# Performance work log

Measured on AMD Instinct MI355X. Metric: run time of the kernel, lower is better.

Reference implementation:

```python
import jax, jax.numpy as jnp
import numpy as np

NB_LAYERS, KSIZE = 4, 5
DILATIONS = [1, 2, 4, 8]
NEG_SLOPE = 0.1
BN_EPS = 1e-5


def _cont_conv(times, feats, mask, dilation, p):
    """One ContConv1d layer: causal gather of time-diffs -> kernel MLP -> weighted aggregate + skip + BN."""
    k1W, k1b, k2W, k2b, k3W, k3b, skipW, skipb, gamma, beta = p
    bs, L, Cin = feats.shape
    Cout = skipW.shape[1]
    lags = jnp.arange(KSIZE) * dilation                    # (K,) include_zero_lag=True -> lag 0 included
    idx = jnp.arange(L)[None, :] - lags[:, None]           # (K, L) causal neighbor indices
    valid = idx >= 0
    idx_c = jnp.clip(idx, 0, L - 1)
    g_times = times[:, idx_c]                              # (bs, K, L)
    g_feats = feats[:, idx_c, :]                           # (bs, K, L, Cin)
    g_mask = (mask[:, idx_c] & valid[None] & mask[:, None, :]).astype(feats.dtype)
    dt = (times[:, None, :] - g_times) * g_mask            # (bs, K, L) zeroed where invalid
    # kernel MLP: scalar time-diff -> (Cin, Cout) mixing matrix
    h = jax.nn.leaky_relu(dt[..., None] @ k1W + k1b, NEG_SLOPE)
    h = jax.nn.leaky_relu(h @ k2W + k2b, NEG_SLOPE)
    kv = (h @ k3W + k3b).reshape(bs, KSIZE, L, Cin, Cout) * g_mask[..., None, None]
    out = jnp.einsum('bklc,bklcd->bld', g_feats, kv)       # aggregate over taps and input channels
    out = out + feats @ skipW + skipb                      # 1x1-conv skip connection
    mu = out.mean((0, 1))                                  # BatchNorm1d (training-mode batch stats)
    var = out.var((0, 1))
    return (out - mu) * jax.lax.rsqrt(var + BN_EPS) * gamma + beta


def _ccnn_forward(event_times, event_types, emb, k1W, k1b, k2W, k2b, k3W, k3b, skipW, skipb, gamma, beta):
    bs = event_times.shape[0]
    emb = emb.at[0].set(0.0)                               # padding_idx = 0
    times = jnp.concatenate([jnp.zeros((bs, 1), event_times.dtype), event_times], axis=1)
    bos = jnp.full((bs, 1), jnp.max(event_types) + 1, dtype=event_types.dtype)
    types = jnp.concatenate([bos, event_types], axis=1)
    mask = times != 0                                      # BOS (t=0) masked, as in the original
    enc = emb[types]                                       # (bs, L+1, C)
    for i in range(NB_LAYERS):
        p = (k1W[i], k1b[i], k2W[i], k2b[i], k3W[i], k3b[i], skipW[i], skipb[i], gamma[i], beta[i])
        enc = jax.nn.leaky_relu(_cont_conv(times, enc, mask, DILATIONS[i], p), NEG_SLOPE)
    return enc


def setup_inputs() -> dict:
    key = jax.random.key(0)
    ks = jax.random.split(key, 12)
    bs, L, C, H, num_types = 8, 2048, 32, 16, 100
    s = 0.05
    gaps = jax.random.uniform(ks[0], (bs, L)) * 0.1 + 0.01
    times = jnp.cumsum(gaps, axis=1)                       # strictly increasing positive event times
    types = jax.random.randint(ks[1], (bs, L), 0, num_types) + 1   # 1..num_types
    pad = jnp.arange(L) >= int(0.9 * L)
    times = jnp.where(pad[None, :], 0.0, times).astype(jnp.float32)
    types = jnp.where(pad[None, :], 0, types).astype(jnp.int32)
    return {
        'event_times': times,
        'event_types': types,
        'emb': jax.random.normal(ks[2], (num_types + 2, C)) * s,
        'k1W': jax.random.normal(ks[3], (NB_LAYERS, 1, H)) * s,
        'k1b': jnp.zeros((NB_LAYERS, H)),
        'k2W': jax.random.normal(ks[4], (NB_LAYERS, H, H)) * s,
        'k2b': jnp.zeros((NB_LAYERS, H)),
        'k3W': jax.random.normal(ks[5], (NB_LAYERS, H, C * C)) * s,
        'k3b': jnp.zeros((NB_LAYERS, C * C)),
        'skipW': jax.random.normal(ks[6], (NB_LAYERS, C, C)) * s,
        'skipb': jnp.zeros((NB_LAYERS, C)),
        'gamma': jnp.ones((NB_LAYERS, C)),
        'beta': jnp.zeros((NB_LAYERS, C)),
    }


def reference(event_times, event_types, emb, k1W, k1b, k2W, k2b, k3W, k3b, skipW, skipb, gamma, beta):
    return _ccnn_forward(event_times, event_types, emb, k1W, k1b, k2W, k2b, k3W, k3b, skipW, skipb, gamma, beta)
```

## Files before the change

### kernel.cpp

```cpp
#include <hip/hip_runtime.h>
#include <stdint.h>

#define NB_LAYERS 4
#define KSIZE 5
#define BSZ 8
#define LIN 2048
#define LSEQ 2049
#define CCH 32
#define HCH 16
#define MROWS (BSZ*LSEQ)
#define NTILES ((MROWS+15)/16)
#define NEG 0.1f
#define BNEPS 1e-5f
#define CONVGRID 205
#define CONVBLK 320
#define NFRAG 36
#define WT_HALVES (NFRAG*64*8)

typedef _Float16 h2v __attribute__((ext_vector_type(2)));
typedef _Float16 h8v __attribute__((ext_vector_type(8)));
typedef float    f4v __attribute__((ext_vector_type(4)));

union H8 { h8v v; h2v h[4]; };

static __device__ __forceinline__ h2v mkh2(float a, float b) {
  h2v r; r[0] = (_Float16)a; r[1] = (_Float16)b; return r;
}

static __device__ __forceinline__ void wt_decode(
    int g, const float* __restrict__ k3Wl, const float* __restrict__ k3bl,
    const float* __restrict__ skipWl, int& halfidx, float& val) {
  int n, k;
  if (g < 16384)      { n = g & 31; int c = (g >> 5) & 31; int h = g >> 10; k = h * 32 + c; val = k3Wl[g]; }
  else if (g < 17408) { int g2 = g - 16384; n = g2 & 31; int c = g2 >> 5; k = 512 + c; val = k3bl[g2]; }
  else                { int g2 = g - 17408; n = g2 & 31; int c = g2 >> 5; k = 544 + c; val = skipWl[g2]; }
  int m = n & 15, a = n >> 4, qq = (k >> 3) & 3, hh = k & 7;
  int f = (k < 512) ? ((k >> 5) * 2 + a) : ((k < 544) ? (32 + a) : (34 + a));
  halfidx = f * 512 + ((qq << 4) | m) * 8 + hh;
}

template<int MODE>
__global__ __launch_bounds__(CONVBLK) void conv_kernel(
    const float* __restrict__ enc_in,
    const int*   __restrict__ types,
    const float* __restrict__ emb,
    float* __restrict__ enc_out,
    const float* __restrict__ etimes,
    const float* __restrict__ k1Wp, const float* __restrict__ k1bp,
    const float* __restrict__ k2Wp, const float* __restrict__ k2bp,
    const float* __restrict__ k3W, const float* __restrict__ k3b,
    const float* __restrict__ skipW,
    _Float16* __restrict__ WtG,
    const float* __restrict__ stats_prev,
    const float* __restrict__ partials_prev,
    float* __restrict__ stats_out,
    float* __restrict__ partials_out,
    float* __restrict__ stats_zero,
    const float* __restrict__ gamma_prev, const float* __restrict__ beta_prev,
    int dil)
{
  __shared__ h8v Wl[NFRAG * 64];
  __shared__ h8v swh[(CONVBLK/64) * KSIZE * 16 * 2];
  __shared__ alignas(16) float sW[304];
  __shared__ float sst[64];
  __shared__ float sbn[64];

  const int tid  = threadIdx.x;
  const int lane = tid & 63;
  const int wv   = tid >> 6;
  const int m    = lane & 15;
  const int q    = lane >> 4;

  if (tid < 64) sst[tid] = 0.f;
  if (tid < 16) { sW[tid] = k1Wp[tid]; sW[16 + tid] = k1bp[tid]; sW[32 + tid] = k2bp[tid]; }
  if (tid >= 64) sW[48 + tid - 64] = k2Wp[tid - 64];

  if (MODE == 0) {
    if (blockIdx.x == 0 && tid < 192) stats_zero[tid] = 0.f;
    for (int g = tid; g < WT_HALVES; g += CONVBLK) {
      int hi; float val;
      wt_decode(g, k3W, k3b, skipW, hi, val);
      ((_Float16*)Wl)[hi] = (_Float16)val;
    }
    int id2 = blockIdx.x * CONVBLK + tid;
    if (id2 < 3 * WT_HALVES) {
      int layer = 1 + id2 / WT_HALVES;
      int g = id2 - (layer - 1) * WT_HALVES;
      int hi; float val;
      wt_decode(g, k3W + layer * 16384, k3b + layer * 1024, skipW + layer * 1024, hi, val);
      WtG[(layer - 1) * WT_HALVES + hi] = (_Float16)val;
    }
  } else {
    const float4* src = (const float4*)WtG;
    float4* dst = (float4*)Wl;
    for (int i = tid; i < WT_HALVES / 8; i += CONVBLK) dst[i] = src[i];
    if (partials_prev && tid < 64) sbn[tid] = 0.f;
  }
  __syncthreads();

  if (MODE == 1 && partials_prev) {
    float v = 0.f;
    for (int i = tid; i < CONVGRID * 64; i += CONVBLK) v += partials_prev[i];
    atomicAdd(&sbn[tid & 63], v);
    __syncthreads();
  }

  float sc8[8], ob8[8];
  if (MODE == 1) {
    const float inv = 1.f / (float)MROWS;
#pragma unroll
    for (int j = 0; j < 8; j++) {
      int c = q * 8 + j;
      float s1 = partials_prev ? sbn[c]      : stats_prev[c];
      float s2 = partials_prev ? sbn[32 + c] : stats_prev[32 + c];
      float mu = s1 * inv;
      float var = s2 * inv - mu * mu;
      float sc = gamma_prev[c] * rsqrtf(var + BNEPS);
      sc8[j] = sc; ob8[j] = beta_prev[c] - mu * sc;
    }
  }

  const int tile = blockIdx.x * (CONVBLK / 64) + wv;
  int row = tile * 16 + m;
  bool rvalid = row < MROWS;
  int rowc = min(row, MROWS - 1);
  int b = rowc / LSEQ, pos = rowc % LSEQ;
  float t_l = (pos == 0) ? 0.f : etimes[b * LIN + pos - 1];
  bool mask_l = rvalid && (t_l != 0.f);

  int bosv = 0;
  if (MODE == 0) {
    if (__ballot(pos == 0)) {
      int mx = 0;
#pragma unroll 8
      for (int i = lane; i < BSZ * LIN; i += 64) mx = max(mx, types[i]);
#pragma unroll
      for (int off = 32; off; off >>= 1) mx = max(mx, __shfl_xor(mx, off, 64));
      bosv = mx + 1;
    }
  }

  int jcs[KSIZE]; float tjv[KSIZE];
#pragma unroll
  for (int tap = 0; tap < KSIZE; tap++) {
    int j = pos - tap * dil;
    int jc = max(j, 0); jcs[tap] = jc;
    tjv[tap] = (jc == 0) ? 0.f : etimes[b * LIN + jc - 1];
  }
  float4 fa[KSIZE], fbv[KSIZE];
  int tts[KSIZE];
  if (MODE == 0) {
#pragma unroll
    for (int tap = 0; tap < KSIZE; tap++) {
      int jc = jcs[tap];
      tts[tap] = (jc > 0) ? types[b * LIN + jc - 1] : ((tap == 0) ? bosv : 0);
    }
#pragma unroll
    for (int tap = 0; tap < KSIZE; tap++) {
      const float* ep = emb + tts[tap] * CCH + q * 8;
      fa[tap] = *(const float4*)ep; fbv[tap] = *(const float4*)(ep + 4);
    }
  } else {
#pragma unroll
    for (int tap = 0; tap < KSIZE; tap++) {
      const float* fp = enc_in + (b * LSEQ + jcs[tap]) * CCH + q * 8;
      fa[tap] = *(const float4*)fp; fbv[tap] = *(const float4*)(fp + 4);
    }
  }

  h2v fh[KSIZE][4];
  h2v fself[4];
  float Fb[8];
#pragma unroll
  for (int jj = 0; jj < 8; jj++) Fb[jj] = 0.f;

#pragma unroll
  for (int tap = 0; tap < KSIZE; tap++) {
    bool gm = mask_l && (pos - tap * dil >= 0) && (tjv[tap] != 0.f);
    float fv[8] = {fa[tap].x, fa[tap].y, fa[tap].z, fa[tap].w,
                   fbv[tap].x, fbv[tap].y, fbv[tap].z, fbv[tap].w};
    if (MODE == 0) {
      float zf = (tts[tap] != 0) ? 1.f : 0.f;
#pragma unroll
      for (int jj = 0; jj < 8; jj++) fv[jj] *= zf;
    } else {
#pragma unroll
      for (int jj = 0; jj < 8; jj++) {
        float x = fmaf(fv[jj], sc8[jj], ob8[jj]);
        fv[jj] = fmaxf(x, NEG * x);
      }
    }
    if (tap == 0) {
      float rv = rvalid ? 1.f : 0.f;
#pragma unroll
      for (int p2 = 0; p2 < 4; p2++) fself[p2] = mkh2(fv[2*p2] * rv, fv[2*p2+1] * rv);
    }
    float g = gm ? 1.f : 0.f;
#pragma unroll
    for (int jj = 0; jj < 8; jj++) Fb[jj] += g * fv[jj];
#pragma unroll
    for (int p2 = 0; p2 < 4; p2++) fh[tap][p2] = mkh2(fv[2*p2], fv[2*p2+1]);
  }

#pragma unroll
  for (int rep = 0; rep < 2; rep++) {
    const int jt = rep ? (KSIZE - 1) : (lane >> 4);
    const bool act = rep ? (lane < 16) : true;
    int j2 = pos - jt * dil;
    int jc2 = max(j2, 0);
    float tj2 = (jc2 == 0) ? 0.f : etimes[b * LIN + jc2 - 1];
    bool g2 = act && mask_l && (j2 >= 0) && (tj2 != 0.f);
    float dt = g2 ? (t_l - tj2) : 0.f;

    H8 w0, w1;
    if (__ballot(g2)) {
      const f4v* k1wv = (const f4v*)&sW[0];
      const f4v* k1bv = (const f4v*)&sW[16];
      const f4v* k2bv = (const f4v*)&sW[32];
      float h1[HCH], h2[HCH];
#pragma unroll
      for (int h4 = 0; h4 < 4; h4++) {
        f4v cw = k1wv[h4], cb = k1bv[h4], c2 = k2bv[h4];
#pragma unroll
        for (int r = 0; r < 4; r++) {
          float x = fmaf(dt, cw[r], cb[r]);
          h1[h4*4+r] = fmaxf(x, NEG * x);
          h2[h4*4+r] = c2[r];
        }
      }
#pragma unroll
      for (int hp = 0; hp < HCH; hp++) {
        float hv = h1[hp];
        const f4v* kk = (const f4v*)&sW[48 + hp * 16];
#pragma unroll
        for (int h4 = 0; h4 < 4; h4++) {
          f4v c = kk[h4];
#pragma unroll
          for (int r = 0; r < 4; r++) h2[h4*4+r] = fmaf(hv, c[r], h2[h4*4+r]);
        }
      }
      float g = g2 ? 1.f : 0.f;
#pragma unroll
      for (int p2 = 0; p2 < 4; p2++) {
        float a0 = h2[2*p2];     a0 = fmaxf(a0, NEG * a0) * g;
        float a1 = h2[2*p2+1];   a1 = fmaxf(a1, NEG * a1) * g;
        w0.h[p2] = mkh2(a0, a1);
        float b0 = h2[8+2*p2];   b0 = fmaxf(b0, NEG * b0) * g;
        float b1 = h2[8+2*p2+1]; b1 = fmaxf(b1, NEG * b1) * g;
        w1.h[p2] = mkh2(b0, b1);
      }
    } else {
#pragma unroll
      for (int p2 = 0; p2 < 4; p2++) { w0.h[p2] = mkh2(0.f, 0.f); w1.h[p2] = mkh2(0.f, 0.f); }
    }
    if (act) {
      int base = ((wv * KSIZE + jt) * 16 + m) * 2;
      swh[base] = w0.v; swh[base + 1] = w1.v;
    }
  }
  __syncthreads();

  h2v wh[KSIZE][8];
#pragma unroll
  for (int tap = 0; tap < KSIZE; tap++) {
    int base = ((wv * KSIZE + tap) * 16 + m) * 2;
    H8 a0, a1; a0.v = swh[base]; a1.v = swh[base + 1];
#pragma unroll
    for (int p2 = 0; p2 < 4; p2++) { wh[tap][p2] = a0.h[p2]; wh[tap][4+p2] = a1.h[p2]; }
  }

  f4v aP = {0,0,0,0}, aQ = {0,0,0,0}, bP = {0,0,0,0}, bQ = {0,0,0,0};

#pragma unroll
  for (int ks = 0; ks < 16; ks++) {
    H8 bf0, bf1, af;
    bf0.v = Wl[(2*ks + 0) * 64 + lane];
    bf1.v = Wl[(2*ks + 1) * 64 + lane];
    h2v u0 = mkh2(0.f,0.f), u1 = mkh2(0.f,0.f), u2 = mkh2(0.f,0.f), u3 = mkh2(0.f,0.f);
#pragma unroll
    for (int tap = 0; tap < KSIZE; tap++) {
      _Float16 w = wh[tap][ks >> 1][ks & 1];
      h2v wd; wd[0] = w; wd[1] = w;
      u0 += wd * fh[tap][0];
      u1 += wd * fh[tap][1];
      u2 += wd * fh[tap][2];
      u3 += wd * fh[tap][3];
    }
    af.h[0] = u0; af.h[1] = u1; af.h[2] = u2; af.h[3] = u3;
    if (ks & 1) {
      aQ = __builtin_amdgcn_mfma_f32_16x16x32_f16(af.v, bf0.v, aQ, 0, 0, 0);
      bQ = __builtin_amdgcn_mfma_f32_16x16x32_f16(af.v, bf1.v, bQ, 0, 0, 0);
    } else {
      aP = __builtin_amdgcn_mfma_f32_16x16x32_f16(af.v, bf0.v, aP, 0, 0, 0);
      bP = __builtin_amdgcn_mfma_f32_16x16x32_f16(af.v, bf1.v, bP, 0, 0, 0);
    }
  }
  {
    H8 bf0, bf1, af;
    bf0.v = Wl[32 * 64 + lane];
    bf1.v = Wl[33 * 64 + lane];
#pragma unroll
    for (int p2 = 0; p2 < 4; p2++) af.h[p2] = mkh2(Fb[2*p2], Fb[2*p2+1]);
    aP = __builtin_amdgcn_mfma_f32_16x16x32_f16(af.v, bf0.v, aP, 0, 0, 0);
    bP = __builtin_amdgcn_mfma_f32_16x16x32_f16(af.v, bf1.v, bP, 0, 0, 0);
  }
  {
    H8 bf0, bf1, af;
    bf0.v = Wl[34 * 64 + lane];
    bf1.v = Wl[35 * 64 + lane];
    af.h[0] = fself[0]; af.h[1] = fself[1]; af.h[2] = fself[2]; af.h[3] = fself[3];
    aQ = __builtin_amdgcn_mfma_f32_16x16x32_f16(af.v, bf0.v, aQ, 0, 0, 0);
    bQ = __builtin_amdgcn_mfma_f32_16x16x32_f16(af.v, bf1.v, bQ, 0, 0, 0);
  }
  f4v acc0 = aP + aQ;
  f4v acc1 = bP + bQ;

  float s0 = 0.f, s1 = 0.f, s2 = 0.f, s3 = 0.f;
#pragma unroll
  for (int r = 0; r < 4; r++) {
    float v0 = acc0[r], v1 = acc1[r];
    s0 += v0; s1 += v0 * v0; s2 += v1; s3 += v1 * v1;
    int rd = tile * 16 + q * 4 + r;
    if (rd < MROWS) {
      enc_out[rd * CCH + m] = v0;
      enc_out[rd * CCH + 16 + m] = v1;
    }
  }
  s0 += __shfl_xor(s0, 16, 64); s0 += __shfl_xor(s0, 32, 64);
  s1 += __shfl_xor(s1, 16, 64); s1 += __shfl_xor(s1, 32, 64);
  s2 += __shfl_xor(s2, 16, 64); s2 += __shfl_xor(s2, 32, 64);
  s3 += __shfl_xor(s3, 16, 64); s3 += __shfl_xor(s3, 32, 64);
  if (q == 0) {
    atomicAdd(&sst[m], s0);
    atomicAdd(&sst[32 + m], s1);
    atomicAdd(&sst[16 + m], s2);
    atomicAdd(&sst[48 + m], s3);
  }
  __syncthreads();
  if (tid < 64) {
    if (MODE == 0) partials_out[blockIdx.x * 64 + tid] = sst[tid];
    else           atomicAdd(&stats_out[tid], sst[tid]);
  }
}

__global__ __launch_bounds__(256) void bn_kernel(
    const float* __restrict__ x, float* __restrict__ out,
    const float* __restrict__ stats,
    const float* __restrict__ gamma, const float* __restrict__ beta) {
  int id = blockIdx.x * blockDim.x + threadIdx.x;
  int c = id & 31;
  const float inv = 1.f / (float)MROWS;
  float mu = stats[c] * inv;
  float var = stats[32 + c] * inv - mu * mu;
  float sc = gamma[c] * rsqrtf(var + BNEPS);
  float v = fmaf(x[id], sc, beta[c] - mu * sc);
  out[id] = fmaxf(v, NEG * v);
}

extern "C" void kernel_launch(void* const* d_in, const int* in_sizes, int n_in,
                              void* d_out, int out_size, void* d_ws, size_t ws_size,
                              hipStream_t stream) {
  (void)in_sizes; (void)n_in; (void)out_size; (void)ws_size;
  const float* event_times = (const float*)d_in[0];
  const int*   event_types = (const int*)d_in[1];
  const float* emb   = (const float*)d_in[2];
  const float* k1W   = (const float*)d_in[3];
  const float* k1b   = (const float*)d_in[4];
  const float* k2W   = (const float*)d_in[5];
  const float* k2b   = (const float*)d_in[6];
  const float* k3W   = (const float*)d_in[7];
  const float* k3b   = (const float*)d_in[8];
  const float* skipW = (const float*)d_in[9];
  const float* gamma = (const float*)d_in[11];
  const float* beta  = (const float*)d_in[12];

  float* enc_a = (float*)d_ws;
  float* enc_b = enc_a + (size_t)MROWS * CCH;
  float* stats = enc_b + (size_t)MROWS * CCH;
  float* partials0 = stats + NB_LAYERS * 64;
  _Float16* WtG = (_Float16*)(((uintptr_t)(partials0 + CONVGRID * 64) + 255) & ~(uintptr_t)255);

  conv_kernel<0><<<CONVGRID, CONVBLK, 0, stream>>>(
      nullptr, event_types, emb, enc_b, event_times,
      k1W, k1b, k2W, k2b, k3W, k3b, skipW, WtG,
      nullptr, nullptr, nullptr, partials0, stats + 64,
      nullptr, nullptr, 1);

  conv_kernel<1><<<CONVGRID, CONVBLK, 0, stream>>>(
      enc_b, nullptr, nullptr, enc_a, event_times,
      k1W + HCH, k1b + HCH, k2W + HCH*HCH, k2b + HCH,
      nullptr, nullptr, nullptr, WtG + 0 * WT_HALVES,
      nullptr, partials0, stats + 64, nullptr, nullptr,
      gamma + 0 * CCH, beta + 0 * CCH, 2);

  conv_kernel<1><<<CONVGRID, CONVBLK, 0, stream>>>(
      enc_a, nullptr, nullptr, enc_b, event_times,
      k1W + 2*HCH, k1b + 2*HCH, k2W + 2*HCH*HCH, k2b + 2*HCH,
      nullptr, nullptr, nullptr, WtG + 1 * WT_HALVES,
      stats + 64, nullptr, stats + 128, nullptr, nullptr,
      gamma + 1 * CCH, beta + 1 * CCH, 4);

  conv_kernel<1><<<CONVGRID, CONVBLK, 0, stream>>>(
      enc_b, nullptr, nullptr, enc_a, event_times,
      k1W + 3*HCH, k1b + 3*HCH, k2W + 3*HCH*HCH, k2b + 3*HCH,
      nullptr, nullptr, nullptr, WtG + 2 * WT_HALVES,
      stats + 128, nullptr, stats + 192, nullptr, nullptr,
      gamma + 2 * CCH, beta + 2 * CCH, 8);

  bn_kernel<<<2049, 256, 0, stream>>>(enc_a, (float*)d_out,
      stats + 192, gamma + 3 * CCH, beta + 3 * CCH);
}
```

Baseline: 165.6 us.

## Fuse all layers into one cooperative persistent kernel with grid barriers

Replaces the five separate launches (four conv layers and the final BN) with one cooperative kernel that runs every layer back to back, separated by a software sense-reversing grid barrier. Weight packing and the per-wave type max for the BOS token are done once up front. Each wave now reads the B fragments directly from global memory instead of first staging the weights in LDS. The aim is to remove launch gaps and the per-block LDS weight copy, at the cost of grid-wide barrier spins, an extra memset, and B operands coming from global or L2.

```diff
diff --git a/kernel.cpp b/kernel.cpp
--- a/kernel.cpp
+++ b/kernel.cpp
@@ -10,12 +10,14 @@
 #define HCH 16
 #define MROWS (BSZ*LSEQ)
 #define NTILES ((MROWS+15)/16)
+#define KDIM 576
 #define NEG 0.1f
 #define BNEPS 1e-5f
-#define CONVGRID 205
-#define CONVBLK 320
-#define NFRAG 36
-#define WT_HALVES (NFRAG*64*8)
+#define NWAVEMAX 256
+#define GRID 205
+#define BLOCK 320
+#define NWAVES (BLOCK/64)
+#define NTHREADS (GRID*BLOCK)
 
 typedef _Float16 h2v __attribute__((ext_vector_type(2)));
 typedef _Float16 h8v __attribute__((ext_vector_type(8)));
@@ -27,83 +29,55 @@
   h2v r; r[0] = (_Float16)a; r[1] = (_Float16)b; return r;
 }
 
-static __device__ __forceinline__ void wt_decode(
-    int g, const float* __restrict__ k3Wl, const float* __restrict__ k3bl,
-    const float* __restrict__ skipWl, int& halfidx, float& val) {
-  int n, k;
-  if (g < 16384)      { n = g & 31; int c = (g >> 5) & 31; int h = g >> 10; k = h * 32 + c; val = k3Wl[g]; }
-  else if (g < 17408) { int g2 = g - 16384; n = g2 & 31; int c = g2 >> 5; k = 512 + c; val = k3bl[g2]; }
-  else                { int g2 = g - 17408; n = g2 & 31; int c = g2 >> 5; k = 544 + c; val = skipWl[g2]; }
-  int m = n & 15, a = n >> 4, qq = (k >> 3) & 3, hh = k & 7;
-  int f = (k < 512) ? ((k >> 5) * 2 + a) : ((k < 544) ? (32 + a) : (34 + a));
-  halfidx = f * 512 + ((qq << 4) | m) * 8 + hh;
+struct CParams {
+  const float* etimes; const int* types; const float* emb;
+  const float* k1W; const float* k1b; const float* k2W; const float* k2b;
+  const float* k3W; const float* k3b; const float* skipW;
+  const float* gamma; const float* beta;
+  float* enc_a; float* enc_b; float* stats; int* wavemax;
+  int* barmem;
+  _Float16* Wt; float* out;
+};
+
+static __device__ __forceinline__ void gbar(int* cnt, int* sense, int epoch) {
+  __syncthreads();
+  if (threadIdx.x == 0) {
+    __threadfence();
+    int prev = __hip_atomic_fetch_add(cnt, 1, __ATOMIC_ACQ_REL, __HIP_MEMORY_SCOPE_AGENT);
+    if (prev == GRID - 1) {
+      __hip_atomic_store(cnt, 0, __ATOMIC_RELAXED, __HIP_MEMORY_SCOPE_AGENT);
+      __hip_atomic_store(sense, epoch, __ATOMIC_RELEASE, __HIP_MEMORY_SCOPE_AGENT);
+    } else {
+      while (__hip_atomic_load(sense, __ATOMIC_ACQUIRE, __HIP_MEMORY_SCOPE_AGENT) < epoch)
+        __builtin_amdgcn_s_sleep(1);
+    }
+    __threadfence();
+  }
+  __syncthreads();
 }
 
 template<int MODE>
-__global__ __launch_bounds__(CONVBLK) void conv_kernel(
-    const float* __restrict__ enc_in,
-    const int*   __restrict__ types,
-    const float* __restrict__ emb,
-    float* __restrict__ enc_out,
-    const float* __restrict__ etimes,
+static __device__ __forceinline__ void conv_layer(
+    const CParams& P, int bid,
+    const float* __restrict__ enc_in, float* __restrict__ enc_out,
     const float* __restrict__ k1Wp, const float* __restrict__ k1bp,
     const float* __restrict__ k2Wp, const float* __restrict__ k2bp,
-    const float* __restrict__ k3W, const float* __restrict__ k3b,
-    const float* __restrict__ skipW,
-    _Float16* __restrict__ WtG,
-    const float* __restrict__ stats_prev,
-    const float* __restrict__ partials_prev,
-    float* __restrict__ stats_out,
-    float* __restrict__ partials_out,
-    float* __restrict__ stats_zero,
+    const _Float16* __restrict__ WtL,
+    const float* __restrict__ stats_prev, float* __restrict__ stats_out,
     const float* __restrict__ gamma_prev, const float* __restrict__ beta_prev,
-    int dil)
+    int dil, float* sW, h8v* swh, float* sst)
 {
-  __shared__ h8v Wl[NFRAG * 64];
-  __shared__ h8v swh[(CONVBLK/64) * KSIZE * 16 * 2];
-  __shared__ alignas(16) float sW[304];
-  __shared__ float sst[64];
-  __shared__ float sbn[64];
-
   const int tid  = threadIdx.x;
   const int lane = tid & 63;
   const int wv   = tid >> 6;
   const int m    = lane & 15;
   const int q    = lane >> 4;
+  const float* etimes = P.etimes;
 
   if (tid < 64) sst[tid] = 0.f;
   if (tid < 16) { sW[tid] = k1Wp[tid]; sW[16 + tid] = k1bp[tid]; sW[32 + tid] = k2bp[tid]; }
   if (tid >= 64) sW[48 + tid - 64] = k2Wp[tid - 64];
-
-  if (MODE == 0) {
-    if (blockIdx.x == 0 && tid < 192) stats_zero[tid] = 0.f;
-    for (int g = tid; g < WT_HALVES; g += CONVBLK) {
-      int hi; float val;
-      wt_decode(g, k3W, k3b, skipW, hi, val);
-      ((_Float16*)Wl)[hi] = (_Float16)val;
-    }
-    int id2 = blockIdx.x * CONVBLK + tid;
-    if (id2 < 3 * WT_HALVES) {
-      int layer = 1 + id2 / WT_HALVES;
-      int g = id2 - (layer - 1) * WT_HALVES;
-      int hi; float val;
-      wt_decode(g, k3W + layer * 16384, k3b + layer * 1024, skipW + layer * 1024, hi, val);
-      WtG[(layer - 1) * WT_HALVES + hi] = (_Float16)val;
-    }
-  } else {
-    const float4* src = (const float4*)WtG;
-    float4* dst = (float4*)Wl;
-    for (int i = tid; i < WT_HALVES / 8; i += CONVBLK) dst[i] = src[i];
-    if (partials_prev && tid < 64) sbn[tid] = 0.f;
-  }
   __syncthreads();
-
-  if (MODE == 1 && partials_prev) {
-    float v = 0.f;
-    for (int i = tid; i < CONVGRID * 64; i += CONVBLK) v += partials_prev[i];
-    atomicAdd(&sbn[tid & 63], v);
-    __syncthreads();
-  }
 
   float sc8[8], ob8[8];
   if (MODE == 1) {
@@ -111,16 +85,17 @@
 #pragma unroll
     for (int j = 0; j < 8; j++) {
       int c = q * 8 + j;
-      float s1 = partials_prev ? sbn[c]      : stats_prev[c];
-      float s2 = partials_prev ? sbn[32 + c] : stats_prev[32 + c];
-      float mu = s1 * inv;
-      float var = s2 * inv - mu * mu;
+      float mu = stats_prev[c] * inv;
+      float var = stats_prev[32 + c] * inv - mu * mu;
       float sc = gamma_prev[c] * rsqrtf(var + BNEPS);
       sc8[j] = sc; ob8[j] = beta_prev[c] - mu * sc;
     }
   }
 
-  const int tile = blockIdx.x * (CONVBLK / 64) + wv;
+  const _Float16* wb0 = WtL + m * KDIM + q * 8;
+  const _Float16* wb1 = WtL + (m + 16) * KDIM + q * 8;
+
+  const int tile = bid * NWAVES + wv;
   int row = tile * 16 + m;
   bool rvalid = row < MROWS;
   int rowc = min(row, MROWS - 1);
@@ -131,11 +106,13 @@
   int bosv = 0;
   if (MODE == 0) {
     if (__ballot(pos == 0)) {
+      const int4* wm = (const int4*)P.wavemax;
       int mx = 0;
-#pragma unroll 8
-      for (int i = lane; i < BSZ * LIN; i += 64) mx = max(mx, types[i]);
-#pragma unroll
-      for (int off = 32; off; off >>= 1) mx = max(mx, __shfl_xor(mx, off, 64));
+#pragma unroll 4
+      for (int i = 0; i < NWAVEMAX / 4; i++) {
+        int4 v = wm[i];
+        mx = max(mx, max(max(v.x, v.y), max(v.z, v.w)));
+      }
       bosv = mx + 1;
     }
   }
@@ -153,11 +130,11 @@
 #pragma unroll
     for (int tap = 0; tap < KSIZE; tap++) {
       int jc = jcs[tap];
-      tts[tap] = (jc > 0) ? types[b * LIN + jc - 1] : ((tap == 0) ? bosv : 0);
+      tts[tap] = (jc > 0) ? P.types[b * LIN + jc - 1] : ((tap == 0) ? bosv : 0);
     }
 #pragma unroll
     for (int tap = 0; tap < KSIZE; tap++) {
-      const float* ep = emb + tts[tap] * CCH + q * 8;
+      const float* ep = P.emb + tts[tap] * CCH + q * 8;
       fa[tap] = *(const float4*)ep; fbv[tap] = *(const float4*)(ep + 4);
     }
   } else {
@@ -274,8 +251,8 @@
 #pragma unroll
   for (int ks = 0; ks < 16; ks++) {
     H8 bf0, bf1, af;
-    bf0.v = Wl[(2*ks + 0) * 64 + lane];
-    bf1.v = Wl[(2*ks + 1) * 64 + lane];
+    bf0.v = *(const h8v*)(wb0 + ks * 32);
+    bf1.v = *(const h8v*)(wb1 + ks * 32);
     h2v u0 = mkh2(0.f,0.f), u1 = mkh2(0.f,0.f), u2 = mkh2(0.f,0.f), u3 = mkh2(0.f,0.f);
 #pragma unroll
     for (int tap = 0; tap < KSIZE; tap++) {
@@ -297,8 +274,8 @@
   }
   {
     H8 bf0, bf1, af;
-    bf0.v = Wl[32 * 64 + lane];
-    bf1.v = Wl[33 * 64 + lane];
+    bf0.v = *(const h8v*)(wb0 + 512);
+    bf1.v = *(const h8v*)(wb1 + 512);
 #pragma unroll
     for (int p2 = 0; p2 < 4; p2++) af.h[p2] = mkh2(Fb[2*p2], Fb[2*p2+1]);
     aP = __builtin_amdgcn_mfma_f32_16x16x32_f16(af.v, bf0.v, aP, 0, 0, 0);
@@ -306,8 +283,8 @@
   }
   {
     H8 bf0, bf1, af;
-    bf0.v = Wl[34 * 64 + lane];
-    bf1.v = Wl[35 * 64 + lane];
+    bf0.v = *(const h8v*)(wb0 + 544);
+    bf1.v = *(const h8v*)(wb1 + 544);
     af.h[0] = fself[0]; af.h[1] = fself[1]; af.h[2] = fself[2]; af.h[3] = fself[3];
     aQ = __builtin_amdgcn_mfma_f32_16x16x32_f16(af.v, bf0.v, aQ, 0, 0, 0);
     bQ = __builtin_amdgcn_mfma_f32_16x16x32_f16(af.v, bf1.v, bQ, 0, 0, 0);
@@ -337,76 +314,109 @@
     atomicAdd(&sst[48 + m], s3);
   }
   __syncthreads();
-  if (tid < 64) {
-    if (MODE == 0) partials_out[blockIdx.x * 64 + tid] = sst[tid];
-    else           atomicAdd(&stats_out[tid], sst[tid]);
-  }
+  if (tid < 64) atomicAdd(&stats_out[tid], sst[tid]);
 }
 
-__global__ __launch_bounds__(256) void bn_kernel(
-    const float* __restrict__ x, float* __restrict__ out,
-    const float* __restrict__ stats,
-    const float* __restrict__ gamma, const float* __restrict__ beta) {
-  int id = blockIdx.x * blockDim.x + threadIdx.x;
-  int c = id & 31;
-  const float inv = 1.f / (float)MROWS;
-  float mu = stats[c] * inv;
-  float var = stats[32 + c] * inv - mu * mu;
-  float sc = gamma[c] * rsqrtf(var + BNEPS);
-  float v = fmaf(x[id], sc, beta[c] - mu * sc);
-  out[id] = fmaxf(v, NEG * v);
+__global__ __launch_bounds__(BLOCK, 1) void ccnn_kernel(CParams P) {
+  __shared__ alignas(16) float sW[304];
+  __shared__ h8v swh[NWAVES * KSIZE * 16 * 2];
+  __shared__ float sst[64];
+
+  const int tid = threadIdx.x;
+  const int bid = blockIdx.x;
+  const int gtid = bid * BLOCK + tid;
+  int* cnt = P.barmem;
+  int* sense = P.barmem + 1;
+
+  if (bid == 0 && tid < NB_LAYERS * 64) P.stats[tid] = 0.f;
+  if (gtid < BSZ * LIN) {
+    int v = P.types[gtid];
+#pragma unroll
+    for (int off = 32; off; off >>= 1) v = max(v, __shfl_xor(v, off, 64));
+    if ((tid & 63) == 0) P.wavemax[gtid >> 6] = v;
+  }
+  for (int id = gtid; id < NB_LAYERS * CCH * KDIM; id += NTHREADS) {
+    int layer = id / (CCH * KDIM);
+    int rem = id % (CCH * KDIM);
+    int n = rem / KDIM;
+    int k = rem % KDIM;
+    float val;
+    if (k < 512)      { int h = k >> 5, c = k & 31; val = P.k3W[layer*16384 + h*1024 + c*32 + n]; }
+    else if (k < 544) { int c = k - 512;            val = P.k3b[layer*1024 + c*32 + n]; }
+    else              { int c = k - 544;            val = P.skipW[layer*1024 + c*32 + n]; }
+    P.Wt[id] = (_Float16)val;
+  }
+  gbar(cnt, sense, 1);
+
+  conv_layer<0>(P, bid, nullptr, P.enc_b,
+      P.k1W, P.k1b, P.k2W, P.k2b, P.Wt,
+      nullptr, P.stats, nullptr, nullptr, 1, sW, swh, sst);
+  gbar(cnt, sense, 2);
+
+  conv_layer<1>(P, bid, P.enc_b, P.enc_a,
+      P.k1W + HCH, P.k1b + HCH, P.k2W + HCH*HCH, P.k2b + HCH,
+      P.Wt + 1 * CCH * KDIM,
+      P.stats, P.stats + 64, P.gamma, P.beta, 2, sW, swh, sst);
+  gbar(cnt, sense, 3);
+
+  conv_layer<1>(P, bid, P.enc_a, P.enc_b,
+      P.k1W + 2*HCH, P.k1b + 2*HCH, P.k2W + 2*HCH*HCH, P.k2b + 2*HCH,
+      P.Wt + 2 * CCH * KDIM,
+      P.stats + 64, P.stats + 128, P.gamma + CCH, P.beta + CCH, 4, sW, swh, sst);
+  gbar(cnt, sense, 4);
+
+  conv_layer<1>(P, bid, P.enc_b, P.enc_a,
+      P.k1W + 3*HCH, P.k1b + 3*HCH, P.k2W + 3*HCH*HCH, P.k2b + 3*HCH,
+      P.Wt + 3 * CCH * KDIM,
+      P.stats + 128, P.stats + 192, P.gamma + 2*CCH, P.beta + 2*CCH, 8, sW, swh, sst);
+  gbar(cnt, sense, 5);
+
+  {
+    const float* st = P.stats + 3 * 64;
+    const int c = gtid & 31;
+    const float inv = 1.f / (float)MROWS;
+    float mu = st[c] * inv;
+    float var = st[32 + c] * inv - mu * mu;
+    float sc = P.gamma[3 * CCH + c] * rsqrtf(var + BNEPS);
+    float ob = P.beta[3 * CCH + c] - mu * sc;
+    for (int id = gtid; id < MROWS * CCH; id += NTHREADS) {
+      float v = fmaf(P.enc_a[id], sc, ob);
+      P.out[id] = fmaxf(v, NEG * v);
+    }
+  }
 }
 
 extern "C" void kernel_launch(void* const* d_in, const int* in_sizes, int n_in,
                               void* d_out, int out_size, void* d_ws, size_t ws_size,
                               hipStream_t stream) {
   (void)in_sizes; (void)n_in; (void)out_size; (void)ws_size;
-  const float* event_times = (const float*)d_in[0];
-  const int*   event_types = (const int*)d_in[1];
-  const float* emb   = (const float*)d_in[2];
-  const float* k1W   = (const float*)d_in[3];
-  const float* k1b   = (const float*)d_in[4];
-  const float* k2W   = (const float*)d_in[5];
-  const float* k2b   = (const float*)d_in[6];
-  const float* k3W   = (const float*)d_in[7];
-  const float* k3b   = (const float*)d_in[8];
-  const float* skipW = (const float*)d_in[9];
-  const float* gamma = (const float*)d_in[11];
-  const float* beta  = (const float*)d_in[12];
+  CParams p;
+  p.etimes = (const float*)d_in[0];
+  p.types  = (const int*)d_in[1];
+  p.emb    = (const float*)d_in[2];
+  p.k1W    = (const float*)d_in[3];
+  p.k1b    = (const float*)d_in[4];
+  p.k2W    = (const float*)d_in[5];
+  p.k2b    = (const float*)d_in[6];
+  p.k3W    = (const float*)d_in[7];
+  p.k3b    = (const float*)d_in[8];
+  p.skipW  = (const float*)d_in[9];
+  p.gamma  = (const float*)d_in[11];
+  p.beta   = (const float*)d_in[12];
 
   float* enc_a = (float*)d_ws;
   float* enc_b = enc_a + (size_t)MROWS * CCH;
   float* stats = enc_b + (size_t)MROWS * CCH;
-  float* partials0 = stats + NB_LAYERS * 64;
-  _Float16* WtG = (_Float16*)(((uintptr_t)(partials0 + CONVGRID * 64) + 255) & ~(uintptr_t)255);
-
-  conv_kernel<0><<<CONVGRID, CONVBLK, 0, stream>>>(
-      nullptr, event_types, emb, enc_b, event_times,
-      k1W, k1b, k2W, k2b, k3W, k3b, skipW, WtG,
-      nullptr, nullptr, nullptr, partials0, stats + 64,
-      nullptr, nullptr, 1);
-
-  conv_kernel<1><<<CONVGRID, CONVBLK, 0, stream>>>(
-      enc_b, nullptr, nullptr, enc_a, event_times,
-      k1W + HCH, k1b + HCH, k2W + HCH*HCH, k2b + HCH,
-      nullptr, nullptr, nullptr, WtG + 0 * WT_HALVES,
-      nullptr, partials0, stats + 64, nullptr, nullptr,
-      gamma + 0 * CCH, beta + 0 * CCH, 2);
-
-  conv_kernel<1><<<CONVGRID, CONVBLK, 0, stream>>>(
-      enc_a, nullptr, nullptr, enc_b, event_times,
-      k1W + 2*HCH, k1b + 2*HCH, k2W + 2*HCH*HCH, k2b + 2*HCH,
-      nullptr, nullptr, nullptr, WtG + 1 * WT_HALVES,
-      stats + 64, nullptr, stats + 128, nullptr, nullptr,
-      gamma + 1 * CCH, beta + 1 * CCH, 4);
-
-  conv_kernel<1><<<CONVGRID, CONVBLK, 0, stream>>>(
-      enc_b, nullptr, nullptr, enc_a, event_times,
-      k1W + 3*HCH, k1b + 3*HCH, k2W + 3*HCH*HCH, k2b + 3*HCH,
-      nullptr, nullptr, nullptr, WtG + 2 * WT_HALVES,
-      stats + 128, nullptr, stats + 192, nullptr, nullptr,
-      gamma + 2 * CCH, beta + 2 * CCH, 8);
-
-  bn_kernel<<<2049, 256, 0, stream>>>(enc_a, (float*)d_out,
-      stats + 192, gamma + 3 * CCH, beta + 3 * CCH);
+  int* wavemax = (int*)(stats + NB_LAYERS * 64);
+  int* barmem  = wavemax + NWAVEMAX;
+  _Float16* Wt = (_Float16*)(((uintptr_t)(barmem + 4) + 255) & ~(uintptr_t)255);
+
+  p.enc_a = enc_a; p.enc_b = enc_b; p.stats = stats; p.wavemax = wavemax;
+  p.barmem = barmem; p.Wt = Wt; p.out = (float*)d_out;
+
+  hipMemsetAsync(barmem, 0, 16, stream);
+
+  void* kargs[] = { (void*)&p };
+  hipLaunchCooperativeKernel((const void*)ccnn_kernel, dim3(GRID), dim3(BLOCK),
+                             kargs, 0, stream);
 }
```

After: 280.7 us. +69.6%, slower.

## Read mixing weights directly from global in later layers, shrink blocks to 256

Applied to the files above, without the earlier changes.

Layers 1-3 of the conv kernel no longer stage the 36-fragment fp16 weight matrix into LDS. Each MFMA B-fragment is loaded straight from global memory, which removes the per-block copy and the 36 KB LDS footprint and should raise occupancy. Blocks shrink from 320 to 256 threads with a 257-block grid. Fully out-of-range tiles skip the compute but still hit a matching barrier. The BOS max-type scan now uses int4 loads. The trade-off is more global/L2 traffic for weight fragments per wave.

```diff
diff --git a/kernel.cpp b/kernel.cpp
--- a/kernel.cpp
+++ b/kernel.cpp
@@ -12,8 +12,8 @@
 #define NTILES ((MROWS+15)/16)
 #define NEG 0.1f
 #define BNEPS 1e-5f
-#define CONVGRID 205
-#define CONVBLK 320
+#define GRID 257
+#define BLK 256
 #define NFRAG 36
 #define WT_HALVES (NFRAG*64*8)
 
@@ -40,7 +40,7 @@
 }
 
 template<int MODE>
-__global__ __launch_bounds__(CONVBLK) void conv_kernel(
+__global__ __launch_bounds__(BLK) void conv_kernel(
     const float* __restrict__ enc_in,
     const int*   __restrict__ types,
     const float* __restrict__ emb,
@@ -59,8 +59,8 @@
     const float* __restrict__ gamma_prev, const float* __restrict__ beta_prev,
     int dil)
 {
-  __shared__ h8v Wl[NFRAG * 64];
-  __shared__ h8v swh[(CONVBLK/64) * KSIZE * 16 * 2];
+  __shared__ h8v Wl[(MODE == 0) ? (NFRAG * 64) : 1];
+  __shared__ h8v swh[(BLK/64) * KSIZE * 16 * 2];
   __shared__ alignas(16) float sW[304];
   __shared__ float sst[64];
   __shared__ float sbn[64];
@@ -73,16 +73,16 @@
 
   if (tid < 64) sst[tid] = 0.f;
   if (tid < 16) { sW[tid] = k1Wp[tid]; sW[16 + tid] = k1bp[tid]; sW[32 + tid] = k2bp[tid]; }
-  if (tid >= 64) sW[48 + tid - 64] = k2Wp[tid - 64];
+  sW[48 + tid] = k2Wp[tid];
 
   if (MODE == 0) {
     if (blockIdx.x == 0 && tid < 192) stats_zero[tid] = 0.f;
-    for (int g = tid; g < WT_HALVES; g += CONVBLK) {
+    for (int g = tid; g < WT_HALVES; g += BLK) {
       int hi; float val;
       wt_decode(g, k3W, k3b, skipW, hi, val);
       ((_Float16*)Wl)[hi] = (_Float16)val;
     }
-    int id2 = blockIdx.x * CONVBLK + tid;
+    int id2 = blockIdx.x * BLK + tid;
     if (id2 < 3 * WT_HALVES) {
       int layer = 1 + id2 / WT_HALVES;
       int g = id2 - (layer - 1) * WT_HALVES;
@@ -91,16 +91,13 @@
       WtG[(layer - 1) * WT_HALVES + hi] = (_Float16)val;
     }
   } else {
-    const float4* src = (const float4*)WtG;
-    float4* dst = (float4*)Wl;
-    for (int i = tid; i < WT_HALVES / 8; i += CONVBLK) dst[i] = src[i];
     if (partials_prev && tid < 64) sbn[tid] = 0.f;
   }
   __syncthreads();
 
   if (MODE == 1 && partials_prev) {
     float v = 0.f;
-    for (int i = tid; i < CONVGRID * 64; i += CONVBLK) v += partials_prev[i];
+    for (int i = tid; i < GRID * 64; i += BLK) v += partials_prev[i];
     atomicAdd(&sbn[tid & 63], v);
     __syncthreads();
   }
@@ -120,221 +117,242 @@
     }
   }
 
-  const int tile = blockIdx.x * (CONVBLK / 64) + wv;
-  int row = tile * 16 + m;
-  bool rvalid = row < MROWS;
-  int rowc = min(row, MROWS - 1);
-  int b = rowc / LSEQ, pos = rowc % LSEQ;
-  float t_l = (pos == 0) ? 0.f : etimes[b * LIN + pos - 1];
-  bool mask_l = rvalid && (t_l != 0.f);
-
-  int bosv = 0;
-  if (MODE == 0) {
-    if (__ballot(pos == 0)) {
-      int mx = 0;
-#pragma unroll 8
-      for (int i = lane; i < BSZ * LIN; i += 64) mx = max(mx, types[i]);
-#pragma unroll
-      for (int off = 32; off; off >>= 1) mx = max(mx, __shfl_xor(mx, off, 64));
-      bosv = mx + 1;
-    }
-  }
-
-  int jcs[KSIZE]; float tjv[KSIZE];
-#pragma unroll
-  for (int tap = 0; tap < KSIZE; tap++) {
-    int j = pos - tap * dil;
-    int jc = max(j, 0); jcs[tap] = jc;
-    tjv[tap] = (jc == 0) ? 0.f : etimes[b * LIN + jc - 1];
-  }
-  float4 fa[KSIZE], fbv[KSIZE];
-  int tts[KSIZE];
-  if (MODE == 0) {
+  const int tile = blockIdx.x * (BLK / 64) + wv;
+  const bool deadtile = (tile * 16 >= MROWS);
+
+  if (!deadtile) {
+    int row = tile * 16 + m;
+    bool rvalid = row < MROWS;
+    int rowc = min(row, MROWS - 1);
+    int b = rowc / LSEQ, pos = rowc % LSEQ;
+    float t_l = (pos == 0) ? 0.f : etimes[b * LIN + pos - 1];
+    bool mask_l = rvalid && (t_l != 0.f);
+
+    int bosv = 0;
+    if (MODE == 0) {
+      if (__ballot(pos == 0)) {
+        const int4* tp = (const int4*)types;
+        int mx = 0;
+#pragma unroll 4
+        for (int i = lane; i < (BSZ * LIN) / 4; i += 64) {
+          int4 v = tp[i];
+          mx = max(mx, max(max(v.x, v.y), max(v.z, v.w)));
+        }
+#pragma unroll
+        for (int off = 32; off; off >>= 1) mx = max(mx, __shfl_xor(mx, off, 64));
+        bosv = mx + 1;
+      }
+    }
+
+    int jcs[KSIZE]; float tjv[KSIZE];
 #pragma unroll
     for (int tap = 0; tap < KSIZE; tap++) {
-      int jc = jcs[tap];
-      tts[tap] = (jc > 0) ? types[b * LIN + jc - 1] : ((tap == 0) ? bosv : 0);
-    }
+      int j = pos - tap * dil;
+      int jc = max(j, 0); jcs[tap] = jc;
+      tjv[tap] = (jc == 0) ? 0.f : etimes[b * LIN + jc - 1];
+    }
+    float4 fa[KSIZE], fbv[KSIZE];
+    int tts[KSIZE];
+    if (MODE == 0) {
+#pragma unroll
+      for (int tap = 0; tap < KSIZE; tap++) {
+        int jc = jcs[tap];
+        tts[tap] = (jc > 0) ? types[b * LIN + jc - 1] : ((tap == 0) ? bosv : 0);
+      }
+#pragma unroll
+      for (int tap = 0; tap < KSIZE; tap++) {
+        const float* ep = emb + tts[tap] * CCH + q * 8;
+        fa[tap] = *(const float4*)ep; fbv[tap] = *(const float4*)(ep + 4);
+      }
+    } else {
+#pragma unroll
+      for (int tap = 0; tap < KSIZE; tap++) {
+        const float* fp = enc_in + (b * LSEQ + jcs[tap]) * CCH + q * 8;
+        fa[tap] = *(const float4*)fp; fbv[tap] = *(const float4*)(fp + 4);
+      }
+    }
+
+    h2v fh[KSIZE][4];
+    h2v fself[4];
+    float Fb[8];
+#pragma unroll
+    for (int jj = 0; jj < 8; jj++) Fb[jj] = 0.f;
+
 #pragma unroll
     for (int tap = 0; tap < KSIZE; tap++) {
-      const float* ep = emb + tts[tap] * CCH + q * 8;
-      fa[tap] = *(const float4*)ep; fbv[tap] = *(const float4*)(ep + 4);
-    }
-  } else {
+      bool gm = mask_l && (pos - tap * dil >= 0) && (tjv[tap] != 0.f);
+      float fv[8] = {fa[tap].x, fa[tap].y, fa[tap].z, fa[tap].w,
+                     fbv[tap].x, fbv[tap].y, fbv[tap].z, fbv[tap].w};
+      if (MODE == 0) {
+        float zf = (tts[tap] != 0) ? 1.f : 0.f;
+#pragma unroll
+        for (int jj = 0; jj < 8; jj++) fv[jj] *= zf;
+      } else {
+#pragma unroll
+        for (int jj = 0; jj < 8; jj++) {
+          float x = fmaf(fv[jj], sc8[jj], ob8[jj]);
+          fv[jj] = fmaxf(x, NEG * x);
+        }
+      }
+      if (tap == 0) {
+        float rv = rvalid ? 1.f : 0.f;
+#pragma unroll
+        for (int p2 = 0; p2 < 4; p2++) fself[p2] = mkh2(fv[2*p2] * rv, fv[2*p2+1] * rv);
+      }
+      float g = gm ? 1.f : 0.f;
+#pragma unroll
+      for (int jj = 0; jj < 8; jj++) Fb[jj] += g * fv[jj];
+#pragma unroll
+      for (int p2 = 0; p2 < 4; p2++) fh[tap][p2] = mkh2(fv[2*p2], fv[2*p2+1]);
+    }
+
+#pragma unroll
+    for (int rep = 0; rep < 2; rep++) {
+      const int jt = rep ? (KSIZE - 1) : (lane >> 4);
+      const bool act = rep ? (lane < 16) : true;
+      int j2 = pos - jt * dil;
+      int jc2 = max(j2, 0);
+      float tj2 = (jc2 == 0) ? 0.f : etimes[b * LIN + jc2 - 1];
+      bool g2 = act && mask_l && (j2 >= 0) && (tj2 != 0.f);
+      float dt = g2 ? (t_l - tj2) : 0.f;
+
+      H8 w0, w1;
+      if (__ballot(g2)) {
+        const f4v* k1wv = (const f4v*)&sW[0];
+        const f4v* k1bv = (const f4v*)&sW[16];
+        const f4v* k2bv = (const f4v*)&sW[32];
+        float h1[HCH], h2[HCH];
+#pragma unroll
+        for (int h4 = 0; h4 < 4; h4++) {
+          f4v cw = k1wv[h4], cb = k1bv[h4], c2 = k2bv[h4];
+#pragma unroll
+          for (int r = 0; r < 4; r++) {
+            float x = fmaf(dt, cw[r], cb[r]);
+            h1[h4*4+r] = fmaxf(x, NEG * x);
+            h2[h4*4+r] = c2[r];
+          }
+        }
+#pragma unroll
+        for (int hp = 0; hp < HCH; hp++) {
+          float hv = h1[hp];
+          const f4v* kk = (const f4v*)&sW[48 + hp * 16];
+#pragma unroll
+          for (int h4 = 0; h4 < 4; h4++) {
+            f4v c = kk[h4];
+#pragma unroll
+            for (int r = 0; r < 4; r++) h2[h4*4+r] = fmaf(hv, c[r], h2[h4*4+r]);
+          }
+        }
+        float g = g2 ? 1.f : 0.f;
+#pragma unroll
+        for (int p2 = 0; p2 < 4; p2++) {
+          float a0 = h2[2*p2];     a0 = fmaxf(a0, NEG * a0) * g;
+          float a1 = h2[2*p2+1];   a1 = fmaxf(a1, NEG * a1) * g;
+          w0.h[p2] = mkh2(a0, a1);
+          float b0 = h2[8+2*p2];   b0 = fmaxf(b0, NEG * b0) * g;
+          float b1 = h2[8+2*p2+1]; b1 = fmaxf(b1, NEG * b1) * g;
+          w1.h[p2] = mkh2(b0, b1);
+        }
+      } else {
+#pragma unroll
+        for (int p2 = 0; p2 < 4; p2++) { w0.h[p2] = mkh2(0.f, 0.f); w1.h[p2] = mkh2(0.f, 0.f); }
+      }
+      if (act) {
+        int base = ((wv * KSIZE + jt) * 16 + m) * 2;
+        swh[base] = w0.v; swh[base + 1] = w1.v;
+      }
+    }
+    __syncthreads();
+
+    h2v wh[KSIZE][8];
 #pragma unroll
     for (int tap = 0; tap < KSIZE; tap++) {
-      const float* fp = enc_in + (b * LSEQ + jcs[tap]) * CCH + q * 8;
-      fa[tap] = *(const float4*)fp; fbv[tap] = *(const float4*)(fp + 4);
-    }
-  }
-
-  h2v fh[KSIZE][4];
-  h2v fself[4];
-  float Fb[8];
-#pragma unroll
-  for (int jj = 0; jj < 8; jj++) Fb[jj] = 0.f;
-
-#pragma unroll
-  for (int tap = 0; tap < KSIZE; tap++) {
-    bool gm = mask_l && (pos - tap * dil >= 0) && (tjv[tap] != 0.f);
-    float fv[8] = {fa[tap].x, fa[tap].y, fa[tap].z, fa[tap].w,
-                   fbv[tap].x, fbv[tap].y, fbv[tap].z, fbv[tap].w};
-    if (MODE == 0) {
-      float zf = (tts[tap] != 0) ? 1.f : 0.f;
-#pragma unroll
-      for (int jj = 0; jj < 8; jj++) fv[jj] *= zf;
-    } else {
-#pragma unroll
-      for (int jj = 0; jj < 8; jj++) {
-        float x = fmaf(fv[jj], sc8[jj], ob8[jj]);
-        fv[jj] = fmaxf(x, NEG * x);
-      }
-    }
-    if (tap == 0) {
-      float rv = rvalid ? 1.f : 0.f;
-#pragma unroll
-      for (int p2 = 0; p2 < 4; p2++) fself[p2] = mkh2(fv[2*p2] * rv, fv[2*p2+1] * rv);
-    }
-    float g = gm ? 1.f : 0.f;
-#pragma unroll
-    for (int jj = 0; jj < 8; jj++) Fb[jj] += g * fv[jj];
-#pragma unroll
-    for (int p2 = 0; p2 < 4; p2++) fh[tap][p2] = mkh2(fv[2*p2], fv[2*p2+1]);
-  }
-
-#pragma unroll
-  for (int rep = 0; rep < 2; rep++) {
-    const int jt = rep ? (KSIZE - 1) : (lane >> 4);
-    const bool act = rep ? (lane < 16) : true;
-    int j2 = pos - jt * dil;
-    int jc2 = max(j2, 0);
-    float tj2 = (jc2 == 0) ? 0.f : etimes[b * LIN + jc2 - 1];
-    bool g2 = act && mask_l && (j2 >= 0) && (tj2 != 0.f);
-    float dt = g2 ? (t_l - tj2) : 0.f;
-
-    H8 w0, w1;
-    if (__ballot(g2)) {
-      const f4v* k1wv = (const f4v*)&sW[0];
-      const f4v* k1bv = (const f4v*)&sW[16];
-      const f4v* k2bv = (const f4v*)&sW[32];
-      float h1[HCH], h2[HCH];
-#pragma unroll
-      for (int h4 = 0; h4 < 4; h4++) {
-        f4v cw = k1wv[h4], cb = k1bv[h4], c2 = k2bv[h4];
-#pragma unroll
-        for (int r = 0; r < 4; r++) {
-          float x = fmaf(dt, cw[r], cb[r]);
-          h1[h4*4+r] = fmaxf(x, NEG * x);
-          h2[h4*4+r] = c2[r];
-        }
-      }
-#pragma unroll
-      for (int hp = 0; hp < HCH; hp++) {
-        float hv = h1[hp];
-        const f4v* kk = (const f4v*)&sW[48 + hp * 16];
-#pragma unroll
-        for (int h4 = 0; h4 < 4; h4++) {
-          f4v c = kk[h4];
-#pragma unroll
-          for (int r = 0; r < 4; r++) h2[h4*4+r] = fmaf(hv, c[r], h2[h4*4+r]);
-        }
-      }
-      float g = g2 ? 1.f : 0.f;
-#pragma unroll
-      for (int p2 = 0; p2 < 4; p2++) {
-        float a0 = h2[2*p2];     a0 = fmaxf(a0, NEG * a0) * g;
-        float a1 = h2[2*p2+1];   a1 = fmaxf(a1, NEG * a1) * g;
-        w0.h[p2] = mkh2(a0, a1);
-        float b0 = h2[8+2*p2];   b0 = fmaxf(b0, NEG * b0) * g;
-        float b1 = h2[8+2*p2+1]; b1 = fmaxf(b1, NEG * b1) * g;
-        w1.h[p2] = mkh2(b0, b1);
-      }
-    } else {
-#pragma unroll
-      for (int p2 = 0; p2 < 4; p2++) { w0.h[p2] = mkh2(0.f, 0.f); w1.h[p2] = mkh2(0.f, 0.f); }
-    }
-    if (act) {
-      int base = ((wv * KSIZE + jt) * 16 + m) * 2;
-      swh[base] = w0.v; swh[base + 1] = w1.v;
-    }
-  }
-  __syncthreads();
-
-  h2v wh[KSIZE][8];
-#pragma unroll
-  for (int tap = 0; tap < KSIZE; tap++) {
-    int base = ((wv * KSIZE + tap) * 16 + m) * 2;
-    H8 a0, a1; a0.v = swh[base]; a1.v = swh[base + 1];
-#pragma unroll
-    for (int p2 = 0; p2 < 4; p2++) { wh[tap][p2] = a0.h[p2]; wh[tap][4+p2] = a1.h[p2]; }
-  }
-
-  f4v aP = {0,0,0,0}, aQ = {0,0,0,0}, bP = {0,0,0,0}, bQ = {0,0,0,0};
-
-#pragma unroll
-  for (int ks = 0; ks < 16; ks++) {
-    H8 bf0, bf1, af;
-    bf0.v = Wl[(2*ks + 0) * 64 + lane];
-    bf1.v = Wl[(2*ks + 1) * 64 + lane];
-    h2v u0 = mkh2(0.f,0.f), u1 = mkh2(0.f,0.f), u2 = mkh2(0.f,0.f), u3 = mkh2(0.f,0.f);
-#pragma unroll
-    for (int tap = 0; tap < KSIZE; tap++) {
-      _Float16 w = wh[tap][ks >> 1][ks & 1];
-      h2v wd; wd[0] = w; wd[1] = w;
-      u0 += wd * fh[tap][0];
-      u1 += wd * fh[tap][1];
-      u2 += wd * fh[tap][2];
-      u3 += wd * fh[tap][3];
-    }
-    af.h[0] = u0; af.h[1] = u1; af.h[2] = u2; af.h[3] = u3;
-    if (ks & 1) {
+      int base = ((wv * KSIZE + tap) * 16 + m) * 2;
+      H8 a0, a1; a0.v = swh[base]; a1.v = swh[base + 1];
+#pragma unroll
+      for (int p2 = 0; p2 < 4; p2++) { wh[tap][p2] = a0.h[p2]; wh[tap][4+p2] = a1.h[p2]; }
+    }
+
+    f4v aP = {0,0,0,0}, aQ = {0,0,0,0}, bP = {0,0,0,0}, bQ = {0,0,0,0};
+
+#pragma unroll
+    for (int ks = 0; ks < 16; ks++) {
+      H8 bf0, bf1, af;
+      if (MODE == 0) {
+        bf0.v = Wl[(2*ks + 0) * 64 + lane];
+        bf1.v = Wl[(2*ks + 1) * 64 + lane];
+      } else {
+        bf0.v = *(const h8v*)(WtG + (size_t)((2*ks + 0) * 64 + lane) * 8);
+        bf1.v = *(const h8v*)(WtG + (size_t)((2*ks + 1) * 64 + lane) * 8);
+      }
+      h2v u0 = mkh2(0.f,0.f), u1 = mkh2(0.f,0.f), u2 = mkh2(0.f,0.f), u3 = mkh2(0.f,0.f);
+#pragma unroll
+      for (int tap = 0; tap < KSIZE; tap++) {
+        _Float16 w = wh[tap][ks >> 1][ks & 1];
+        h2v wd; wd[0] = w; wd[1] = w;
+        u0 += wd * fh[tap][0];
+        u1 += wd * fh[tap][1];
+        u2 += wd * fh[tap][2];
+        u3 += wd * fh[tap][3];
+      }
+      af.h[0] = u0; af.h[1] = u1; af.h[2] = u2; af.h[3] = u3;
+      if (ks & 1) {
+        aQ = __builtin_amdgcn_mfma_f32_16x16x32_f16(af.v, bf0.v, aQ, 0, 0, 0);
+        bQ = __builtin_amdgcn_mfma_f32_16x16x32_f16(af.v, bf1.v, bQ, 0, 0, 0);
+      } else {
+        aP = __builtin_amdgcn_mfma_f32_16x16x32_f16(af.v, bf0.v, aP, 0, 0, 0);
+        bP = __builtin_amdgcn_mfma_f32_16x16x32_f16(af.v, bf1.v, bP, 0, 0, 0);
+      }
+    }
+    {
+      H8 bf0, bf1, af;
+      if (MODE == 0) { bf0.v = Wl[32 * 64 + lane]; bf1.v = Wl[33 * 64 + lane]; }
+      else {
+        bf0.v = *(const h8v*)(WtG + (size_t)(32 * 64 + lane) * 8);
+        bf1.v = *(const h8v*)(WtG + (size_t)(33 * 64 + lane) * 8);
+      }
+#pragma unroll
+      for (int p2 = 0; p2 < 4; p2++) af.h[p2] = mkh2(Fb[2*p2], Fb[2*p2+1]);
+      aP = __builtin_amdgcn_mfma_f32_16x16x32_f16(af.v, bf0.v, aP, 0, 0, 0);
+      bP = __builtin_amdgcn_mfma_f32_16x16x32_f16(af.v, bf1.v, bP, 0, 0, 0);
+    }
+    {
+      H8 bf0, bf1, af;
+      if (MODE == 0) { bf0.v = Wl[34 * 64 + lane]; bf1.v = Wl[35 * 64 + lane]; }
+      else {
+        bf0.v = *(const h8v*)(WtG + (size_t)(34 * 64 + lane) * 8);
+        bf1.v = *(const h8v*)(WtG + (size_t)(35 * 64 + lane) * 8);
+      }
+      af.h[0] = fself[0]; af.h[1] = fself[1]; af.h[2] = fself[2]; af.h[3] = fself[3];
       aQ = __builtin_amdgcn_mfma_f32_16x16x32_f16(af.v, bf0.v, aQ, 0, 0, 0);
       bQ = __builtin_amdgcn_mfma_f32_16x16x32_f16(af.v, bf1.v, bQ, 0, 0, 0);
-    } else {
-      aP = __builtin_amdgcn_mfma_f32_16x16x32_f16(af.v, bf0.v, aP, 0, 0, 0);
-      bP = __builtin_amdgcn_mfma_f32_16x16x32_f16(af.v, bf1.v, bP, 0, 0, 0);
-    }
-  }
-  {
-    H8 bf0, bf1, af;
-    bf0.v = Wl[32 * 64 + lane];
-    bf1.v = Wl[33 * 64 + lane];
-#pragma unroll
-    for (int p2 = 0; p2 < 4; p2++) af.h[p2] = mkh2(Fb[2*p2], Fb[2*p2+1]);
-    aP = __builtin_amdgcn_mfma_f32_16x16x32_f16(af.v, bf0.v, aP, 0, 0, 0);
-    bP = __builtin_amdgcn_mfma_f32_16x16x32_f16(af.v, bf1.v, bP, 0, 0, 0);
-  }
-  {
-    H8 bf0, bf1, af;
-    bf0.v = Wl[34 * 64 + lane];
-    bf1.v = Wl[35 * 64 + lane];
-    af.h[0] = fself[0]; af.h[1] = fself[1]; af.h[2] = fself[2]; af.h[3] = fself[3];
-    aQ = __builtin_amdgcn_mfma_f32_16x16x32_f16(af.v, bf0.v, aQ, 0, 0, 0);
-    bQ = __builtin_amdgcn_mfma_f32_16x16x32_f16(af.v, bf1.v, bQ, 0, 0, 0);
-  }
-  f4v acc0 = aP + aQ;
-  f4v acc1 = bP + bQ;
-
-  float s0 = 0.f, s1 = 0.f, s2 = 0.f, s3 = 0.f;
-#pragma unroll
-  for (int r = 0; r < 4; r++) {
-    float v0 = acc0[r], v1 = acc1[r];
-    s0 += v0; s1 += v0 * v0; s2 += v1; s3 += v1 * v1;
-    int rd = tile * 16 + q * 4 + r;
-    if (rd < MROWS) {
-      enc_out[rd * CCH + m] = v0;
-      enc_out[rd * CCH + 16 + m] = v1;
-    }
-  }
-  s0 += __shfl_xor(s0, 16, 64); s0 += __shfl_xor(s0, 32, 64);
-  s1 += __shfl_xor(s1, 16, 64); s1 += __shfl_xor(s1, 32, 64);
-  s2 += __shfl_xor(s2, 16, 64); s2 += __shfl_xor(s2, 32, 64);
-  s3 += __shfl_xor(s3, 16, 64); s3 += __shfl_xor(s3, 32, 64);
-  if (q == 0) {
-    atomicAdd(&sst[m], s0);
-    atomicAdd(&sst[32 + m], s1);
-    atomicAdd(&sst[16 + m], s2);
-    atomicAdd(&sst[48 + m], s3);
+    }
+    f4v acc0 = aP + aQ;
+    f4v acc1 = bP + bQ;
+
+    float s0 = 0.f, s1 = 0.f, s2 = 0.f, s3 = 0.f;
+#pragma unroll
+    for (int r = 0; r < 4; r++) {
+      float v0 = acc0[r], v1 = acc1[r];
+      s0 += v0; s1 += v0 * v0; s2 += v1; s3 += v1 * v1;
+      int rd = tile * 16 + q * 4 + r;
+      if (rd < MROWS) {
+        enc_out[rd * CCH + m] = v0;
+        enc_out[rd * CCH + 16 + m] = v1;
+      }
+    }
+    s0 += __shfl_xor(s0, 16, 64); s0 += __shfl_xor(s0, 32, 64);
+    s1 += __shfl_xor(s1, 16, 64); s1 += __shfl_xor(s1, 32, 64);
+    s2 += __shfl_xor(s2, 16, 64); s2 += __shfl_xor(s2, 32, 64);
+    s3 += __shfl_xor(s3, 16, 64); s3 += __shfl_xor(s3, 32, 64);
+    if (q == 0) {
+      atomicAdd(&sst[m], s0);
+      atomicAdd(&sst[32 + m], s1);
+      atomicAdd(&sst[16 + m], s2);
+      atomicAdd(&sst[48 + m], s3);
+    }
+  } else {
+    __syncthreads();
   }
   __syncthreads();
   if (tid < 64) {
@@ -378,29 +396,29 @@
   float* enc_b = enc_a + (size_t)MROWS * CCH;
   float* stats = enc_b + (size_t)MROWS * CCH;
   float* partials0 = stats + NB_LAYERS * 64;
-  _Float16* WtG = (_Float16*)(((uintptr_t)(partials0 + CONVGRID * 64) + 255) & ~(uintptr_t)255);
-
-  conv_kernel<0><<<CONVGRID, CONVBLK, 0, stream>>>(
+  _Float16* WtG = (_Float16*)(((uintptr_t)(partials0 + GRID * 64) + 255) & ~(uintptr_t)255);
+
+  conv_kernel<0><<<GRID, BLK, 0, stream>>>(
       nullptr, event_types, emb, enc_b, event_times,
       k1W, k1b, k2W, k2b, k3W, k3b, skipW, WtG,
       nullptr, nullptr, nullptr, partials0, stats + 64,
       nullptr, nullptr, 1);
 
-  conv_kernel<1><<<CONVGRID, CONVBLK, 0, stream>>>(
+  conv_kernel<1><<<GRID, BLK, 0, stream>>>(
       enc_b, nullptr, nullptr, enc_a, event_times,
       k1W + HCH, k1b + HCH, k2W + HCH*HCH, k2b + HCH,
       nullptr, nullptr, nullptr, WtG + 0 * WT_HALVES,
       nullptr, partials0, stats + 64, nullptr, nullptr,
       gamma + 0 * CCH, beta + 0 * CCH, 2);
 
-  conv_kernel<1><<<CONVGRID, CONVBLK, 0, stream>>>(
+  conv_kernel<1><<<GRID, BLK, 0, stream>>>(
       enc_a, nullptr, nullptr, enc_b, event_times,
       k1W + 2*HCH, k1b + 2*HCH, k2W + 2*HCH*HCH, k2b + 2*HCH,
       nullptr, nullptr, nullptr, WtG + 1 * WT_HALVES,
       stats + 64, nullptr, stats + 128, nullptr, nullptr,
       gamma + 1 * CCH, beta + 1 * CCH, 4);
 
-  conv_kernel<1><<<CONVGRID, CONVBLK, 0, stream>>>(
+  conv_kernel<1><<<GRID, BLK, 0, stream>>>(
       enc_b, nullptr, nullptr, enc_a, event_times,
       k1W + 3*HCH, k1b + 3*HCH, k2W + 3*HCH*HCH, k2b + 3*HCH,
       nullptr, nullptr, nullptr, WtG + 2 * WT_HALVES,
```

Measured after the change: 167.7 us. No clear change (+1.3%).
